# Kernel optimization log

Hardware: AMD Instinct MI355X
Metric: run time of the kernel (lower is better)

The kernel has to match this reference:

```python
import jax, jax.numpy as jnp
import numpy as np

V, H, B, S = 32000, 2048, 128, 512
NEG_INF = -1e9

def setup_inputs() -> dict:
    key = jax.random.key(0)
    ks = jax.random.split(key, 12)
    sc = 1.0 / np.sqrt(H)
    embed = jax.random.normal(ks[0], (V, H), jnp.float32) * sc
    embed = embed.at[0].set(0.0)  # padding_idx=0
    return {
        "target_words": jax.random.randint(ks[1], (B,), 0, V),
        "hx": jax.random.normal(ks[2], (B, H), jnp.float32),
        "cx": jax.random.normal(ks[3], (B, H), jnp.float32),
        "ew_hx_list": jax.random.normal(ks[4], (S, B, H), jnp.float32),
        "ew_mask": jax.random.randint(ks[5], (S, B, 1), 0, 2).astype(jnp.int32),
        "embed": embed,
        "W_ih": jax.random.normal(ks[6], (4 * H, H), jnp.float32) * sc,
        "W_hh": jax.random.normal(ks[7], (4 * H, H), jnp.float32) * sc,
        "b_ih": jax.random.normal(ks[8], (4 * H,), jnp.float32) * sc,
        "b_hh": jax.random.normal(ks[9], (4 * H,), jnp.float32) * sc,
        "attn_W": jax.random.normal(ks[10], (H, 2 * H), jnp.float32) * sc,
        "attn_b": jax.random.normal(ks[11], (H,), jnp.float32) * sc,
    }

def reference(target_words, hx, cx, ew_hx_list, ew_mask, embed, W_ih, W_hh, b_ih, b_hh, attn_W, attn_b):
    # forward(): embedding (dropout is identity in eval) + LSTMCell step
    x = embed[target_words]                                   # [B,H]
    gates = x @ W_ih.T + b_ih + hx @ W_hh.T + b_hh            # [B,4H]
    i, f, g, o = jnp.split(gates, 4, axis=-1)                 # PyTorch gate order
    i = jax.nn.sigmoid(i); f = jax.nn.sigmoid(f); o = jax.nn.sigmoid(o)
    g = jnp.tanh(g)
    cx_new = f * cx + i * g
    hx_new = o * jnp.tanh(cx_new)                             # [B,H]
    # attention(): masked dot-score softmax over source dim 0
    scores = jnp.sum(hx_new * ew_hx_list, axis=-1, keepdims=True)  # [S,B,1]
    masked = jnp.where(ew_mask == 0, NEG_INF, scores)
    align = jax.nn.softmax(masked, axis=0)                    # [S,B,1]
    content = jnp.sum(align * ew_hx_list, axis=0)             # [B,H]
    concat = jnp.concatenate([content, hx_new], axis=1)       # [B,2H]
    hx_attention = jnp.tanh(concat @ attn_W.T + attn_b)       # [B,H]
    return hx_attention
```

## Files before the change

kernel.cpp:

```cpp
#include <hip/hip_runtime.h>
#include <math.h>

#define B 128
#define H 2048
#define S 512
#define FOURH 8192
#define LOG2E 1.4426950408889634f

typedef float  f32x4  __attribute__((ext_vector_type(4)));
typedef short  bf16x8 __attribute__((ext_vector_type(8)));
typedef unsigned short u16;
typedef unsigned short u16x8 __attribute__((ext_vector_type(8)));
typedef unsigned short u16x4 __attribute__((ext_vector_type(4)));

__device__ __forceinline__ void cvt_hilo(float x, u16& h, u16& lo) {
    unsigned int u = __float_as_uint(x);
    h = (u16)(u >> 16);
    float hf = __uint_as_float(u & 0xFFFF0000u);
    float r = x - hf;
    lo = (u16)(__float_as_uint(r) >> 16);
}

__global__ __launch_bounds__(256) void gather_convert_A0(
    const int* __restrict__ tw,
    const float* __restrict__ embed,
    const float* __restrict__ hx,
    u16* __restrict__ Ah, u16* __restrict__ Al)
{
    const int i = (blockIdx.x * 256 + threadIdx.x) * 8;
    const int b = i >> 12;
    const int col = i & 4095;
    const float* src = (col < H) ? (embed + (size_t)tw[b] * H + col)
                                 : (hx + (size_t)b * H + (col - H));
    f32x4 v0 = *(const f32x4*)(src);
    f32x4 v1 = *(const f32x4*)(src + 4);
    u16x8 hv, lv;
    #pragma unroll
    for (int j = 0; j < 4; ++j) { u16 h, l; cvt_hilo(v0[j], h, l); hv[j] = h; lv[j] = l; }
    #pragma unroll
    for (int j = 0; j < 4; ++j) { u16 h, l; cvt_hilo(v1[j], h, l); hv[4+j] = h; lv[4+j] = l; }
    *(u16x8*)(Ah + i) = hv;
    *(u16x8*)(Al + i) = lv;
}

template<int MODE>
__global__ __launch_bounds__(256) void split_gemm(
    const u16* __restrict__ Ah, const u16* __restrict__ Al,
    const float* __restrict__ W0, const float* __restrict__ W1,
    float* __restrict__ outp)
{
    constexpr int NOUT = (MODE == 0) ? FOURH : H;
    constexpr int KLEN = (MODE == 0) ? 1024 : 512;
    constexpr int NITER = KLEN / 32;
    __shared__ u16 AhS[128][40];
    __shared__ u16 AlS[128][40];
    __shared__ u16 BhS[32][40];
    __shared__ u16 BlS[32][40];

    const int tid = threadIdx.x;
    const int n0 = blockIdx.x * 32;
    const int kz = blockIdx.y;
    const int kbase = kz * KLEN;
    const int ar = tid >> 1, ac = (tid & 1) * 16;
    const int br = tid >> 3, bc = (tid & 7) * 4;
    const int wv = tid >> 6, lane = tid & 63;
    const int frow = lane & 15, fk = (lane >> 4) * 8, crow = (lane >> 4) * 4;

    const float* Wrow;
    if (MODE == 0)
        Wrow = ((kz < 2) ? W0 : W1) + (size_t)(n0 + br) * H + (kz & 1) * 1024 + bc;
    else
        Wrow = W0 + (size_t)(n0 + br) * (2 * H) + kbase + bc;

    const u16* Abase = Ah + (size_t)ar * 4096 + kbase + ac;
    const u16* Lbase = Al + (size_t)ar * 4096 + kbase + ac;

    f32x4 acc[2][2];
    #pragma unroll
    for (int mi = 0; mi < 2; ++mi)
        #pragma unroll
        for (int ni = 0; ni < 2; ++ni)
            acc[mi][ni] = (f32x4){0.f, 0.f, 0.f, 0.f};

    u16x8 rah0, rah1, ral0, ral1;
    auto loadA = [&](int k0) {
        rah0 = *(const u16x8*)(Abase + k0);
        rah1 = *(const u16x8*)(Abase + k0 + 8);
        ral0 = *(const u16x8*)(Lbase + k0);
        ral1 = *(const u16x8*)(Lbase + k0 + 8);
    };
    auto writeA = [&]() {
        *(u16x8*)&AhS[ar][ac]     = rah0;
        *(u16x8*)&AhS[ar][ac + 8] = rah1;
        *(u16x8*)&AlS[ar][ac]     = ral0;
        *(u16x8*)&AlS[ar][ac + 8] = ral1;
    };
    auto writeB = [&](f32x4 rbv) {
        u16x4 bh, bl;
        #pragma unroll
        for (int j = 0; j < 4; ++j) { u16 h, l; cvt_hilo(rbv[j], h, l); bh[j] = h; bl[j] = l; }
        *(u16x4*)&BhS[br][bc] = bh;
        *(u16x4*)&BlS[br][bc] = bl;
    };
    auto computeTile = [&]() {
        bf16x8 a_h[2], a_l[2], b_h[2], b_l[2];
        #pragma unroll
        for (int mi = 0; mi < 2; ++mi) {
            a_h[mi] = *(const bf16x8*)&AhS[wv * 32 + mi * 16 + frow][fk];
            a_l[mi] = *(const bf16x8*)&AlS[wv * 32 + mi * 16 + frow][fk];
        }
        #pragma unroll
        for (int ni = 0; ni < 2; ++ni) {
            b_h[ni] = *(const bf16x8*)&BhS[ni * 16 + frow][fk];
            b_l[ni] = *(const bf16x8*)&BlS[ni * 16 + frow][fk];
        }
        #pragma unroll
        for (int mi = 0; mi < 2; ++mi)
            #pragma unroll
            for (int ni = 0; ni < 2; ++ni) {
                acc[mi][ni] = __builtin_amdgcn_mfma_f32_16x16x32_bf16(a_h[mi], b_h[ni], acc[mi][ni], 0, 0, 0);
                acc[mi][ni] = __builtin_amdgcn_mfma_f32_16x16x32_bf16(a_h[mi], b_l[ni], acc[mi][ni], 0, 0, 0);
                acc[mi][ni] = __builtin_amdgcn_mfma_f32_16x16x32_bf16(a_l[mi], b_h[ni], acc[mi][ni], 0, 0, 0);
            }
    };

    f32x4 rbvX = *(const f32x4*)(Wrow);
    f32x4 rbvY = *(const f32x4*)(Wrow + 32);
    loadA(0);

    for (int ks = 0; ks < NITER; ks += 2) {
        __syncthreads();
        writeA();
        writeB(rbvX);
        __syncthreads();
        loadA((ks + 1) * 32);
        if (ks + 2 < NITER) rbvX = *(const f32x4*)(Wrow + (ks + 2) * 32);
        computeTile();
        __syncthreads();
        writeA();
        writeB(rbvY);
        __syncthreads();
        if (ks + 2 < NITER) loadA((ks + 2) * 32);
        if (ks + 3 < NITER) rbvY = *(const f32x4*)(Wrow + (ks + 3) * 32);
        computeTile();
    }

    #pragma unroll
    for (int mi = 0; mi < 2; ++mi)
        #pragma unroll
        for (int ni = 0; ni < 2; ++ni) {
            const int col = n0 + ni * 16 + frow;
            #pragma unroll
            for (int j = 0; j < 4; ++j) {
                const int row = wv * 32 + mi * 16 + crow + j;
                outp[((size_t)kz * B + row) * NOUT + col] = acc[mi][ni][j];
            }
        }
}

__global__ __launch_bounds__(256) void lstm_cell(
    const float* __restrict__ gp,
    const float* __restrict__ cx,
    const float* __restrict__ b_ih,
    const float* __restrict__ b_hh,
    float* __restrict__ hxn,
    u16* __restrict__ Ah1, u16* __restrict__ Al1)
{
    const int t = blockIdx.x * 256 + threadIdx.x;
    const int b = t >> 9;
    const int h = (t & 511) * 4;
    const size_t PS = (size_t)B * FOURH;
    const float* g0 = gp + (size_t)b * FOURH;
    f32x4 gi = *(const f32x4*)(b_ih + h)       + *(const f32x4*)(b_hh + h);
    f32x4 gf = *(const f32x4*)(b_ih + H + h)   + *(const f32x4*)(b_hh + H + h);
    f32x4 gg = *(const f32x4*)(b_ih + 2*H + h) + *(const f32x4*)(b_hh + 2*H + h);
    f32x4 go = *(const f32x4*)(b_ih + 3*H + h) + *(const f32x4*)(b_hh + 3*H + h);
    #pragma unroll
    for (int p = 0; p < 4; ++p) {
        gi += *(const f32x4*)(g0 + p * PS + h);
        gf += *(const f32x4*)(g0 + p * PS + H + h);
        gg += *(const f32x4*)(g0 + p * PS + 2*H + h);
        go += *(const f32x4*)(g0 + p * PS + 3*H + h);
    }
    f32x4 cv = *(const f32x4*)(cx + (size_t)b * H + h);
    f32x4 hv;
    #pragma unroll
    for (int j = 0; j < 4; ++j) {
        float i_ = 1.f / (1.f + expf(-gi[j]));
        float f_ = 1.f / (1.f + expf(-gf[j]));
        float o_ = 1.f / (1.f + expf(-go[j]));
        float g_ = tanhf(gg[j]);
        float c_ = f_ * cv[j] + i_ * g_;
        hv[j] = o_ * tanhf(c_);
    }
    *(f32x4*)(hxn + (size_t)b * H + h) = hv;
    u16x4 hh, ll;
    #pragma unroll
    for (int j = 0; j < 4; ++j) { u16 a, l; cvt_hilo(hv[j], a, l); hh[j] = a; ll[j] = l; }
    *(u16x4*)(Ah1 + (size_t)b * 4096 + H + h) = hh;
    *(u16x4*)(Al1 + (size_t)b * 4096 + H + h) = ll;
}

__global__ __launch_bounds__(256) void fused_attn(
    const float* __restrict__ hxn,
    const float* __restrict__ ew,
    const int* __restrict__ mask,
    float* __restrict__ o_part,
    float* __restrict__ ml_part)
{
    __shared__ float mlbuf[4][2];
    __shared__ float obuf[4][2048];

    const int tid = threadIdx.x;
    const int b = blockIdx.x >> 2;
    const int c = blockIdx.x & 3;
    const int wv = tid >> 6;
    const int lane = tid & 63;
    const int s0 = c * 128 + wv * 32;

    unsigned long long mbits;
    {
        int mv = (lane < 32) ? mask[(s0 + lane) * B + b] : 0;
        mbits = __ballot(mv != 0);
    }

    f32x4 hxv[8];
    const float* hp = hxn + (size_t)b * H + lane * 4;
    #pragma unroll
    for (int j = 0; j < 8; ++j) hxv[j] = *(const f32x4*)(hp + j * 256);

    f32x4 o4[8];
    #pragma unroll
    for (int j = 0; j < 8; ++j) o4[j] = (f32x4){0.f, 0.f, 0.f, 0.f};
    float m2 = -3.0e38f, l = 0.f;

    const size_t SSTRIDE = (size_t)B * H;
    const float* rowp = ew + ((size_t)s0 * B + b) * H + lane * 4;

    f32x4 eva[8], evb[8];
    #pragma unroll
    for (int j = 0; j < 8; ++j) eva[j] = *(const f32x4*)(rowp + j * 256);
    #pragma unroll
    for (int j = 0; j < 8; ++j) evb[j] = *(const f32x4*)(rowp + SSTRIDE + j * 256);

    for (int pi = 0; pi < 16; ++pi) {
        f32x4 ca[8], cb[8];
        #pragma unroll
        for (int j = 0; j < 8; ++j) { ca[j] = eva[j]; cb[j] = evb[j]; }
        if (pi < 15) {
            const float* na = rowp + (size_t)(2 * pi + 2) * SSTRIDE;
            const float* nb = rowp + (size_t)(2 * pi + 3) * SSTRIDE;
            #pragma unroll
            for (int j = 0; j < 8; ++j) eva[j] = *(const f32x4*)(na + j * 256);
            #pragma unroll
            for (int j = 0; j < 8; ++j) evb[j] = *(const f32x4*)(nb + j * 256);
        }
        float pa = 0.f, pb = 0.f;
        #pragma unroll
        for (int j = 0; j < 8; ++j) {
            f32x4 ta = ca[j] * hxv[j];
            f32x4 tb = cb[j] * hxv[j];
            pa += ta[0] + ta[1] + ta[2] + ta[3];
            pb += tb[0] + tb[1] + tb[2] + tb[3];
        }
        #pragma unroll
        for (int off = 32; off; off >>= 1) {
            pa += __shfl_xor(pa, off, 64);
            pb += __shfl_xor(pb, off, 64);
        }
        const float p2a = ((mbits >> (2 * pi)) & 1) ? pa * LOG2E : -1.5e9f;
        const float p2b = ((mbits >> (2 * pi + 1)) & 1) ? pb * LOG2E : -1.5e9f;
        const float q = fmaxf(p2a, p2b);
        if (q <= m2) {
            const float ea = exp2f(p2a - m2);
            const float eb = exp2f(p2b - m2);
            l += ea + eb;
            #pragma unroll
            for (int j = 0; j < 8; ++j) o4[j] += ca[j] * ea + cb[j] * eb;
        } else {
            const float sc = exp2f(m2 - q);
            const float ea = exp2f(p2a - q);
            const float eb = exp2f(p2b - q);
            l = l * sc + ea + eb;
            #pragma unroll
            for (int j = 0; j < 8; ++j) o4[j] = o4[j] * sc + ca[j] * ea + cb[j] * eb;
            m2 = q;
        }
    }

    if (lane == 0) { mlbuf[wv][0] = m2; mlbuf[wv][1] = l; }
    __syncthreads();
    const float M = fmaxf(fmaxf(mlbuf[0][0], mlbuf[1][0]), fmaxf(mlbuf[2][0], mlbuf[3][0]));
    const float wsc = exp2f(m2 - M);
    float L = 0.f;
    #pragma unroll
    for (int w = 0; w < 4; ++w) L += mlbuf[w][1] * exp2f(mlbuf[w][0] - M);
    #pragma unroll
    for (int j = 0; j < 8; ++j)
        *(f32x4*)&obuf[wv][j * 256 + lane * 4] = o4[j] * wsc;
    __syncthreads();

    const int h0 = tid * 8;
    f32x4 s0v = (f32x4){0.f, 0.f, 0.f, 0.f}, s1v = s0v;
    #pragma unroll
    for (int w = 0; w < 4; ++w) {
        s0v += *(const f32x4*)&obuf[w][h0];
        s1v += *(const f32x4*)&obuf[w][h0 + 4];
    }
    float* op = o_part + ((size_t)b * 4 + c) * H + h0;
    *(f32x4*)(op)     = s0v;
    *(f32x4*)(op + 4) = s1v;
    if (tid == 0) {
        ml_part[((size_t)b * 4 + c) * 2]     = M;
        ml_part[((size_t)b * 4 + c) * 2 + 1] = L;
    }
}

__global__ __launch_bounds__(256) void attn_combine(
    const float* __restrict__ o_part,
    const float* __restrict__ ml_part,
    u16* __restrict__ Ah1, u16* __restrict__ Al1)
{
    const int b = blockIdx.x;
    const int tid = threadIdx.x;
    float Mc[4], Lc[4];
    #pragma unroll
    for (int c = 0; c < 4; ++c) {
        Mc[c] = ml_part[((size_t)b * 4 + c) * 2];
        Lc[c] = ml_part[((size_t)b * 4 + c) * 2 + 1];
    }
    const float Mg = fmaxf(fmaxf(Mc[0], Mc[1]), fmaxf(Mc[2], Mc[3]));
    float Lg = 0.f;
    #pragma unroll
    for (int c = 0; c < 4; ++c) Lg += Lc[c] * exp2f(Mc[c] - Mg);
    const float inv = 1.f / Lg;
    const int h0 = tid * 8;
    f32x4 a0 = (f32x4){0.f, 0.f, 0.f, 0.f}, a1 = a0;
    #pragma unroll
    for (int c = 0; c < 4; ++c) {
        const float scl = exp2f(Mc[c] - Mg) * inv;
        const float* op = o_part + ((size_t)b * 4 + c) * H + h0;
        a0 += *(const f32x4*)(op) * scl;
        a1 += *(const f32x4*)(op + 4) * scl;
    }
    u16x8 hh, ll;
    #pragma unroll
    for (int j = 0; j < 4; ++j) { u16 a, l; cvt_hilo(a0[j], a, l); hh[j] = a; ll[j] = l; }
    #pragma unroll
    for (int j = 0; j < 4; ++j) { u16 a, l; cvt_hilo(a1[j], a, l); hh[4+j] = a; ll[4+j] = l; }
    *(u16x8*)(Ah1 + (size_t)b * 4096 + h0) = hh;
    *(u16x8*)(Al1 + (size_t)b * 4096 + h0) = ll;
}

__global__ __launch_bounds__(256) void attn_out(
    const float* __restrict__ part,
    const float* __restrict__ attn_b,
    float* __restrict__ out)
{
    const int t = blockIdx.x * 256 + threadIdx.x;
    const int i = t * 4;
    const int n = i & (H - 1);
    const size_t BH = (size_t)B * H;
    f32x4 s = *(const f32x4*)(attn_b + n);
    #pragma unroll
    for (int p = 0; p < 8; ++p) s += *(const f32x4*)(part + p * BH + i);
    f32x4 r;
    #pragma unroll
    for (int j = 0; j < 4; ++j) r[j] = tanhf(s[j]);
    *(f32x4*)(out + i) = r;
}

extern "C" void kernel_launch(void* const* d_in, const int* in_sizes, int n_in,
                              void* d_out, int out_size, void* d_ws, size_t ws_size,
                              hipStream_t stream)
{
    const int*   tw     = (const int*)d_in[0];
    const float* hx     = (const float*)d_in[1];
    const float* cx     = (const float*)d_in[2];
    const float* ew     = (const float*)d_in[3];
    const int*   mask   = (const int*)d_in[4];
    const float* embed  = (const float*)d_in[5];
    const float* W_ih   = (const float*)d_in[6];
    const float* W_hh   = (const float*)d_in[7];
    const float* b_ih   = (const float*)d_in[8];
    const float* b_hh   = (const float*)d_in[9];
    const float* attn_W = (const float*)d_in[10];
    const float* attn_b = (const float*)d_in[11];
    float* out = (float*)d_out;

    float* ws      = (float*)d_ws;
    float* gates_p = ws;
    float* o_part  = gates_p + 4 * (size_t)B * FOURH;
    float* ml      = o_part + (size_t)B * 4 * H;
    float* hxn     = ml + 1024;
    float* out_p   = hxn + (size_t)B * H;
    u16* Ah0 = (u16*)(out_p + 8 * (size_t)B * H);
    u16* Al0 = Ah0 + (size_t)B * 4096;
    u16* Ah1 = Al0 + (size_t)B * 4096;
    u16* Al1 = Ah1 + (size_t)B * 4096;

    gather_convert_A0<<<256, 256, 0, stream>>>(tw, embed, hx, Ah0, Al0);
    split_gemm<0><<<dim3(FOURH / 32, 4), 256, 0, stream>>>(Ah0, Al0, W_ih, W_hh, gates_p);
    lstm_cell<<<256, 256, 0, stream>>>(gates_p, cx, b_ih, b_hh, hxn, Ah1, Al1);
    fused_attn<<<B * 4, 256, 0, stream>>>(hxn, ew, mask, o_part, ml);
    attn_combine<<<B, 256, 0, stream>>>(o_part, ml, Ah1, Al1);
    split_gemm<1><<<dim3(H / 32, 8), 256, 0, stream>>>(Ah1, Al1, attn_W, attn_W, out_p);
    attn_out<<<256, 256, 0, stream>>>(out_p, attn_b, out);
}
```

Baseline: 214.3 us.

## Widen split GEMM tiles to 128x128 per block and double split-K

Measured after the change: 186.0 us, median of 2. -13.2%, faster.

```diff
diff --git a/kernel.cpp b/kernel.cpp
--- a/kernel.cpp
+++ b/kernel.cpp
@@ -50,36 +50,38 @@
     float* __restrict__ outp)
 {
     constexpr int NOUT = (MODE == 0) ? FOURH : H;
-    constexpr int KLEN = (MODE == 0) ? 1024 : 512;
+    constexpr int KLEN = (MODE == 0) ? 512 : 256;
     constexpr int NITER = KLEN / 32;
     __shared__ u16 AhS[128][40];
     __shared__ u16 AlS[128][40];
-    __shared__ u16 BhS[32][40];
-    __shared__ u16 BlS[32][40];
+    __shared__ u16 BhS[128][40];
+    __shared__ u16 BlS[128][40];
 
     const int tid = threadIdx.x;
-    const int n0 = blockIdx.x * 32;
+    const int n0 = blockIdx.x * 128;
     const int kz = blockIdx.y;
     const int kbase = kz * KLEN;
-    const int ar = tid >> 1, ac = (tid & 1) * 16;
-    const int br = tid >> 3, bc = (tid & 7) * 4;
+    const int sr = tid >> 1;
+    const int sc = (tid & 1) * 16;
     const int wv = tid >> 6, lane = tid & 63;
+    const int wr = (wv >> 1) * 64;
+    const int wc = (wv & 1) * 64;
     const int frow = lane & 15, fk = (lane >> 4) * 8, crow = (lane >> 4) * 4;
 
     const float* Wrow;
     if (MODE == 0)
-        Wrow = ((kz < 2) ? W0 : W1) + (size_t)(n0 + br) * H + (kz & 1) * 1024 + bc;
+        Wrow = ((kz < 4) ? W0 : W1) + (size_t)(n0 + sr) * H + (kz & 3) * KLEN + sc;
     else
-        Wrow = W0 + (size_t)(n0 + br) * (2 * H) + kbase + bc;
-
-    const u16* Abase = Ah + (size_t)ar * 4096 + kbase + ac;
-    const u16* Lbase = Al + (size_t)ar * 4096 + kbase + ac;
-
-    f32x4 acc[2][2];
-    #pragma unroll
-    for (int mi = 0; mi < 2; ++mi)
-        #pragma unroll
-        for (int ni = 0; ni < 2; ++ni)
+        Wrow = W0 + (size_t)(n0 + sr) * (2 * H) + kbase + sc;
+
+    const u16* Abase = Ah + (size_t)sr * 4096 + kbase + sc;
+    const u16* Lbase = Al + (size_t)sr * 4096 + kbase + sc;
+
+    f32x4 acc[4][4];
+    #pragma unroll
+    for (int mi = 0; mi < 4; ++mi)
+        #pragma unroll
+        for (int ni = 0; ni < 4; ++ni)
             acc[mi][ni] = (f32x4){0.f, 0.f, 0.f, 0.f};
 
     u16x8 rah0, rah1, ral0, ral1;
@@ -90,69 +92,91 @@
         ral1 = *(const u16x8*)(Lbase + k0 + 8);
     };
     auto writeA = [&]() {
-        *(u16x8*)&AhS[ar][ac]     = rah0;
-        *(u16x8*)&AhS[ar][ac + 8] = rah1;
-        *(u16x8*)&AlS[ar][ac]     = ral0;
-        *(u16x8*)&AlS[ar][ac + 8] = ral1;
-    };
-    auto writeB = [&](f32x4 rbv) {
-        u16x4 bh, bl;
-        #pragma unroll
-        for (int j = 0; j < 4; ++j) { u16 h, l; cvt_hilo(rbv[j], h, l); bh[j] = h; bl[j] = l; }
-        *(u16x4*)&BhS[br][bc] = bh;
-        *(u16x4*)&BlS[br][bc] = bl;
+        *(u16x8*)&AhS[sr][sc]     = rah0;
+        *(u16x8*)&AhS[sr][sc + 8] = rah1;
+        *(u16x8*)&AlS[sr][sc]     = ral0;
+        *(u16x8*)&AlS[sr][sc + 8] = ral1;
+    };
+    f32x4 wX0, wX1, wX2, wX3, wY0, wY1, wY2, wY3;
+    auto loadWX = [&](int k0) {
+        wX0 = *(const f32x4*)(Wrow + k0);
+        wX1 = *(const f32x4*)(Wrow + k0 + 4);
+        wX2 = *(const f32x4*)(Wrow + k0 + 8);
+        wX3 = *(const f32x4*)(Wrow + k0 + 12);
+    };
+    auto loadWY = [&](int k0) {
+        wY0 = *(const f32x4*)(Wrow + k0);
+        wY1 = *(const f32x4*)(Wrow + k0 + 4);
+        wY2 = *(const f32x4*)(Wrow + k0 + 8);
+        wY3 = *(const f32x4*)(Wrow + k0 + 12);
+    };
+    auto writeB = [&](const f32x4& b0, const f32x4& b1,
+                      const f32x4& b2, const f32x4& b3) {
+        u16x8 hv, lv;
+        #pragma unroll
+        for (int j = 0; j < 4; ++j) { u16 h, l; cvt_hilo(b0[j], h, l); hv[j] = h; lv[j] = l; }
+        #pragma unroll
+        for (int j = 0; j < 4; ++j) { u16 h, l; cvt_hilo(b1[j], h, l); hv[4+j] = h; lv[4+j] = l; }
+        *(u16x8*)&BhS[sr][sc] = hv;
+        *(u16x8*)&BlS[sr][sc] = lv;
+        #pragma unroll
+        for (int j = 0; j < 4; ++j) { u16 h, l; cvt_hilo(b2[j], h, l); hv[j] = h; lv[j] = l; }
+        #pragma unroll
+        for (int j = 0; j < 4; ++j) { u16 h, l; cvt_hilo(b3[j], h, l); hv[4+j] = h; lv[4+j] = l; }
+        *(u16x8*)&BhS[sr][sc + 8] = hv;
+        *(u16x8*)&BlS[sr][sc + 8] = lv;
     };
     auto computeTile = [&]() {
-        bf16x8 a_h[2], a_l[2], b_h[2], b_l[2];
-        #pragma unroll
-        for (int mi = 0; mi < 2; ++mi) {
-            a_h[mi] = *(const bf16x8*)&AhS[wv * 32 + mi * 16 + frow][fk];
-            a_l[mi] = *(const bf16x8*)&AlS[wv * 32 + mi * 16 + frow][fk];
-        }
-        #pragma unroll
-        for (int ni = 0; ni < 2; ++ni) {
-            b_h[ni] = *(const bf16x8*)&BhS[ni * 16 + frow][fk];
-            b_l[ni] = *(const bf16x8*)&BlS[ni * 16 + frow][fk];
-        }
-        #pragma unroll
-        for (int mi = 0; mi < 2; ++mi)
-            #pragma unroll
-            for (int ni = 0; ni < 2; ++ni) {
+        bf16x8 a_h[4], a_l[4], b_h[4], b_l[4];
+        #pragma unroll
+        for (int mi = 0; mi < 4; ++mi) {
+            a_h[mi] = *(const bf16x8*)&AhS[wr + mi * 16 + frow][fk];
+            a_l[mi] = *(const bf16x8*)&AlS[wr + mi * 16 + frow][fk];
+        }
+        #pragma unroll
+        for (int ni = 0; ni < 4; ++ni) {
+            b_h[ni] = *(const bf16x8*)&BhS[wc + ni * 16 + frow][fk];
+            b_l[ni] = *(const bf16x8*)&BlS[wc + ni * 16 + frow][fk];
+        }
+        #pragma unroll
+        for (int mi = 0; mi < 4; ++mi)
+            #pragma unroll
+            for (int ni = 0; ni < 4; ++ni) {
                 acc[mi][ni] = __builtin_amdgcn_mfma_f32_16x16x32_bf16(a_h[mi], b_h[ni], acc[mi][ni], 0, 0, 0);
                 acc[mi][ni] = __builtin_amdgcn_mfma_f32_16x16x32_bf16(a_h[mi], b_l[ni], acc[mi][ni], 0, 0, 0);
                 acc[mi][ni] = __builtin_amdgcn_mfma_f32_16x16x32_bf16(a_l[mi], b_h[ni], acc[mi][ni], 0, 0, 0);
             }
     };
 
-    f32x4 rbvX = *(const f32x4*)(Wrow);
-    f32x4 rbvY = *(const f32x4*)(Wrow + 32);
+    loadWX(0);
+    loadWY(32);
     loadA(0);
 
     for (int ks = 0; ks < NITER; ks += 2) {
         __syncthreads();
         writeA();
-        writeB(rbvX);
+        writeB(wX0, wX1, wX2, wX3);
         __syncthreads();
         loadA((ks + 1) * 32);
-        if (ks + 2 < NITER) rbvX = *(const f32x4*)(Wrow + (ks + 2) * 32);
+        if (ks + 2 < NITER) loadWX((ks + 2) * 32);
         computeTile();
         __syncthreads();
         writeA();
-        writeB(rbvY);
+        writeB(wY0, wY1, wY2, wY3);
         __syncthreads();
         if (ks + 2 < NITER) loadA((ks + 2) * 32);
-        if (ks + 3 < NITER) rbvY = *(const f32x4*)(Wrow + (ks + 3) * 32);
+        if (ks + 3 < NITER) loadWY((ks + 3) * 32);
         computeTile();
     }
 
     #pragma unroll
-    for (int mi = 0; mi < 2; ++mi)
-        #pragma unroll
-        for (int ni = 0; ni < 2; ++ni) {
-            const int col = n0 + ni * 16 + frow;
+    for (int mi = 0; mi < 4; ++mi)
+        #pragma unroll
+        for (int ni = 0; ni < 4; ++ni) {
+            const int col = n0 + wc + ni * 16 + frow;
             #pragma unroll
             for (int j = 0; j < 4; ++j) {
-                const int row = wv * 32 + mi * 16 + crow + j;
+                const int row = wr + mi * 16 + crow + j;
                 outp[((size_t)kz * B + row) * NOUT + col] = acc[mi][ni][j];
             }
         }
@@ -176,7 +200,7 @@
     f32x4 gg = *(const f32x4*)(b_ih + 2*H + h) + *(const f32x4*)(b_hh + 2*H + h);
     f32x4 go = *(const f32x4*)(b_ih + 3*H + h) + *(const f32x4*)(b_hh + 3*H + h);
     #pragma unroll
-    for (int p = 0; p < 4; ++p) {
+    for (int p = 0; p < 8; ++p) {
         gi += *(const f32x4*)(g0 + p * PS + h);
         gf += *(const f32x4*)(g0 + p * PS + H + h);
         gg += *(const f32x4*)(g0 + p * PS + 2*H + h);
@@ -363,7 +387,7 @@
     const size_t BH = (size_t)B * H;
     f32x4 s = *(const f32x4*)(attn_b + n);
     #pragma unroll
-    for (int p = 0; p < 8; ++p) s += *(const f32x4*)(part + p * BH + i);
+    for (int p = 0; p < 16; ++p) s += *(const f32x4*)(part + p * BH + i);
     f32x4 r;
     #pragma unroll
     for (int j = 0; j < 4; ++j) r[j] = tanhf(s[j]);
@@ -390,20 +414,20 @@
 
     float* ws      = (float*)d_ws;
     float* gates_p = ws;
-    float* o_part  = gates_p + 4 * (size_t)B * FOURH;
+    float* o_part  = gates_p + 8 * (size_t)B * FOURH;
     float* ml      = o_part + (size_t)B * 4 * H;
     float* hxn     = ml + 1024;
     float* out_p   = hxn + (size_t)B * H;
-    u16* Ah0 = (u16*)(out_p + 8 * (size_t)B * H);
+    u16* Ah0 = (u16*)(out_p + 16 * (size_t)B * H);
     u16* Al0 = Ah0 + (size_t)B * 4096;
     u16* Ah1 = Al0 + (size_t)B * 4096;
     u16* Al1 = Ah1 + (size_t)B * 4096;
 
     gather_convert_A0<<<256, 256, 0, stream>>>(tw, embed, hx, Ah0, Al0);
-    split_gemm<0><<<dim3(FOURH / 32, 4), 256, 0, stream>>>(Ah0, Al0, W_ih, W_hh, gates_p);
+    split_gemm<0><<<dim3(FOURH / 128, 8), 256, 0, stream>>>(Ah0, Al0, W_ih, W_hh, gates_p);
     lstm_cell<<<256, 256, 0, stream>>>(gates_p, cx, b_ih, b_hh, hxn, Ah1, Al1);
     fused_attn<<<B * 4, 256, 0, stream>>>(hxn, ew, mask, o_part, ml);
     attn_combine<<<B, 256, 0, stream>>>(o_part, ml, Ah1, Al1);
-    split_gemm<1><<<dim3(H / 32, 8), 256, 0, stream>>>(Ah1, Al1, attn_W, attn_W, out_p);
+    split_gemm<1><<<dim3(H / 128, 16), 256, 0, stream>>>(Ah1, Al1, attn_W, attn_W, out_p);
     attn_out<<<256, 256, 0, stream>>>(out_p, attn_b, out);
 }
```
